# Optimization experiments

Measured on AMD Instinct MI355X. Metric: run time of the kernel, lower is better.

The kernel has to match this reference:

```python
import jax, jax.numpy as jnp
import numpy as np

# init kwargs baked in as constants
VTH_M = 0.5
VTH_S = 0.1
DECAY_M = 2.0
DECAY_S = 0.1
ALPHA = 4.0

B, T, C, H, W = 16, 32, 64, 32, 32


def spike_fn(x):
    # Heaviside spike; forward only (surrogate gradient used in bwd module)
    return jnp.where(x > 0, 1.0, 0.0).astype(x.dtype)


def setup_inputs() -> dict:
    key = jax.random.key(0)
    k1, k2, k3 = jax.random.split(key, 3)
    x = jax.random.normal(k1, (B, T, C, H, W), dtype=jnp.float32)
    vth_raw = jax.random.normal(k2, (C, H, W), dtype=jnp.float32)
    decay_raw = jax.random.normal(k3, (C, H, W), dtype=jnp.float32)
    return {"x": x, "vth_raw": vth_raw, "decay_raw": decay_raw}


def reference(x, vth_raw, decay_raw):
    # learned per-neuron threshold and decay
    vth = jax.nn.softplus(vth_raw * VTH_S + VTH_M) + 0.01          # (C,H,W)
    decay = jnp.clip(jax.nn.sigmoid(decay_raw * DECAY_S + DECAY_M), 0.0, 0.99)

    x_seq = jnp.moveaxis(x, 1, 0)  # (T, B, C, H, W)

    def scan_fn(v, x_t):
        v = v * decay + x_t                      # leaky integrate
        s = spike_fn(v - vth)                    # fire
        v = v - jax.lax.stop_gradient(s) * vth   # soft reset
        return v, s

    _, spikes = jax.lax.scan(scan_fn, jnp.zeros_like(x_seq[0]), x_seq)
    return jnp.moveaxis(spikes, 0, 1)  # (B, T, C, H, W)
```

## Files before the change

### kernel.cpp

```cpp
#include <hip/hip_runtime.h>
#include <math.h>


#define LIF_B    16
#define LIF_T    32
#define LIF_CHW  65536
#define LIF_CHW2 32768

typedef float vf2 __attribute__((ext_vector_type(2)));

__global__ __launch_bounds__(256) void HR_HLIFLayer2D_kernel(
    const float* __restrict__ x,
    const float* __restrict__ vth_raw,
    const float* __restrict__ decay_raw,
    float* __restrict__ out)
{
    const int g = blockIdx.x * 256 + threadIdx.x;
    const int b = g >> 15;
    const int j = g & (LIF_CHW2 - 1);

    const vf2 vr2 = reinterpret_cast<const vf2*>(vth_raw)[j];
    const vf2 dr2 = reinterpret_cast<const vf2*>(decay_raw)[j];
    const float vrr[2] = {vr2.x, vr2.y};
    const float drr[2] = {dr2.x, dr2.y};

    float vth[2], dec[2];
#pragma unroll
    for (int i = 0; i < 2; ++i) {
        float a  = __fmul_rn(vrr[i], 0.1f);
        float bb = __fadd_rn(a, 0.5f);
        double sp = log1p(exp((double)bb));
        vth[i] = __fadd_rn((float)sp, 0.01f);

        float z = __fmul_rn(drr[i], 0.1f);
        float w = __fadd_rn(z, 2.0f);
        double sg = 1.0 / (1.0 + exp(-(double)w));
        float sgf = (float)sg;
        sgf = fminf(fmaxf(sgf, 0.0f), 0.99f);
        dec[i] = sgf;
    }

    float v[2] = {0.f, 0.f};
    const size_t base2 = (size_t)b * (LIF_T * LIF_CHW2) + (size_t)j;
    const vf2* __restrict__ x2 = reinterpret_cast<const vf2*>(x);
    vf2* __restrict__ o2 = reinterpret_cast<vf2*>(out);

    vf2 xt = x2[base2];
#pragma unroll
    for (int t = 0; t < LIF_T; ++t) {
        const size_t idx = base2 + (size_t)t * LIF_CHW2;
        vf2 xn;
        if (t + 1 < LIF_T) xn = x2[idx + LIF_CHW2];

        const float xi[2] = {xt.x, xt.y};
        vf2 s;
        float so[2];
#pragma unroll
        for (int i = 0; i < 2; ++i) {
            float vv = __fadd_rn(__fmul_rn(v[i], dec[i]), xi[i]);
            float d = __fsub_rn(vv, vth[i]);
            bool fire = (d > 0.0f);
            so[i] = fire ? 1.0f : 0.0f;
            v[i] = fire ? d : vv;
        }
        s.x = so[0]; s.y = so[1];
        __builtin_nontemporal_store(s, &o2[idx]);
        xt = xn;
    }
}

extern "C" void kernel_launch(void* const* d_in, const int* in_sizes, int n_in,
                              void* d_out, int out_size, void* d_ws, size_t ws_size,
                              hipStream_t stream) {
    const float* x         = (const float*)d_in[0];
    const float* vth_raw   = (const float*)d_in[1];
    const float* decay_raw = (const float*)d_in[2];
    float* out             = (float*)d_out;

    const int total_threads = LIF_B * LIF_CHW2;
    const int block = 256;
    const int grid = total_threads / block;
    HR_HLIFLayer2D_kernel<<<grid, block, 0, stream>>>(x, vth_raw, decay_raw, out);
}
```

Measured before the change: 234.3 us.

## Precompute LIF params in a prepass kernel and widen to float4 nontemporal loads

A small prepass kernel computes the per-neuron threshold and decay (double-precision softplus/sigmoid) once into workspace, instead of having every batch thread recompute them. The main kernel then reads the precomputed values, switches from float2 to float4 vector accesses, and uses nontemporal loads for x. The trade-offs are an extra kernel launch, half as many threads (so less parallelism and more registers per thread), and a fallback path that still does the in-kernel computation when the workspace is too small.

```diff
diff --git a/kernel.cpp b/kernel.cpp
--- a/kernel.cpp
+++ b/kernel.cpp
@@ -5,66 +5,85 @@
 #define LIF_B    16
 #define LIF_T    32
 #define LIF_CHW  65536
-#define LIF_CHW2 32768
+#define LIF_CHW4 16384
 
-typedef float vf2 __attribute__((ext_vector_type(2)));
+typedef float vf4 __attribute__((ext_vector_type(4)));
 
+__device__ __forceinline__ float lif_vth_f(float raw) {
+    float a  = __fmul_rn(raw, 0.1f);
+    float bb = __fadd_rn(a, 0.5f);
+    double sp = log1p(exp((double)bb));
+    return __fadd_rn((float)sp, 0.01f);
+}
+
+__device__ __forceinline__ float lif_dec_f(float raw) {
+    float z = __fmul_rn(raw, 0.1f);
+    float w = __fadd_rn(z, 2.0f);
+    double sg = 1.0 / (1.0 + exp(-(double)w));
+    float sgf = (float)sg;
+    return fminf(fmaxf(sgf, 0.0f), 0.99f);
+}
+
+__global__ __launch_bounds__(256) void lif_params_kernel(
+    const float* __restrict__ vth_raw,
+    const float* __restrict__ decay_raw,
+    float* __restrict__ wp)
+{
+    const int i = blockIdx.x * 256 + threadIdx.x;
+    wp[i]           = lif_vth_f(vth_raw[i]);
+    wp[i + LIF_CHW] = lif_dec_f(decay_raw[i]);
+}
+
+template<bool PRE>
 __global__ __launch_bounds__(256) void HR_HLIFLayer2D_kernel(
     const float* __restrict__ x,
-    const float* __restrict__ vth_raw,
-    const float* __restrict__ decay_raw,
+    const float* __restrict__ p_vth,
+    const float* __restrict__ p_dec,
     float* __restrict__ out)
 {
     const int g = blockIdx.x * 256 + threadIdx.x;
-    const int b = g >> 15;
-    const int j = g & (LIF_CHW2 - 1);
+    const int b = g >> 14;
+    const int j = g & (LIF_CHW4 - 1);
 
-    const vf2 vr2 = reinterpret_cast<const vf2*>(vth_raw)[j];
-    const vf2 dr2 = reinterpret_cast<const vf2*>(decay_raw)[j];
-    const float vrr[2] = {vr2.x, vr2.y};
-    const float drr[2] = {dr2.x, dr2.y};
+    const vf4 rv = reinterpret_cast<const vf4*>(p_vth)[j];
+    const vf4 rd = reinterpret_cast<const vf4*>(p_dec)[j];
 
-    float vth[2], dec[2];
+    float vth[4], dec[4];
+    {
+        const float rva[4] = {rv.x, rv.y, rv.z, rv.w};
+        const float rda[4] = {rd.x, rd.y, rd.z, rd.w};
 #pragma unroll
-    for (int i = 0; i < 2; ++i) {
-        float a  = __fmul_rn(vrr[i], 0.1f);
-        float bb = __fadd_rn(a, 0.5f);
-        double sp = log1p(exp((double)bb));
-        vth[i] = __fadd_rn((float)sp, 0.01f);
-
-        float z = __fmul_rn(drr[i], 0.1f);
-        float w = __fadd_rn(z, 2.0f);
-        double sg = 1.0 / (1.0 + exp(-(double)w));
-        float sgf = (float)sg;
-        sgf = fminf(fmaxf(sgf, 0.0f), 0.99f);
-        dec[i] = sgf;
+        for (int i = 0; i < 4; ++i) {
+            vth[i] = PRE ? rva[i] : lif_vth_f(rva[i]);
+            dec[i] = PRE ? rda[i] : lif_dec_f(rda[i]);
+        }
     }
 
-    float v[2] = {0.f, 0.f};
-    const size_t base2 = (size_t)b * (LIF_T * LIF_CHW2) + (size_t)j;
-    const vf2* __restrict__ x2 = reinterpret_cast<const vf2*>(x);
-    vf2* __restrict__ o2 = reinterpret_cast<vf2*>(out);
+    float v[4] = {0.f, 0.f, 0.f, 0.f};
+    const size_t base4 = (size_t)b * (LIF_T * LIF_CHW4) + (size_t)j;
+    const vf4* __restrict__ x4 = reinterpret_cast<const vf4*>(x);
+    vf4* __restrict__ o4 = reinterpret_cast<vf4*>(out);
 
-    vf2 xt = x2[base2];
+    vf4 xt = __builtin_nontemporal_load(&x4[base4]);
 #pragma unroll
     for (int t = 0; t < LIF_T; ++t) {
-        const size_t idx = base2 + (size_t)t * LIF_CHW2;
-        vf2 xn;
-        if (t + 1 < LIF_T) xn = x2[idx + LIF_CHW2];
+        const size_t idx = base4 + (size_t)t * LIF_CHW4;
+        vf4 xn;
+        if (t + 1 < LIF_T)
+            xn = __builtin_nontemporal_load(&x4[idx + LIF_CHW4]);
 
-        const float xi[2] = {xt.x, xt.y};
-        vf2 s;
-        float so[2];
+        const float xi[4] = {xt.x, xt.y, xt.z, xt.w};
+        float so[4];
 #pragma unroll
-        for (int i = 0; i < 2; ++i) {
+        for (int i = 0; i < 4; ++i) {
             float vv = __fadd_rn(__fmul_rn(v[i], dec[i]), xi[i]);
             float d = __fsub_rn(vv, vth[i]);
-            bool fire = (d > 0.0f);
+            const bool fire = (d > 0.0f);
             so[i] = fire ? 1.0f : 0.0f;
             v[i] = fire ? d : vv;
         }
-        s.x = so[0]; s.y = so[1];
-        __builtin_nontemporal_store(s, &o2[idx]);
+        vf4 s; s.x = so[0]; s.y = so[1]; s.z = so[2]; s.w = so[3];
+        __builtin_nontemporal_store(s, &o4[idx]);
         xt = xn;
     }
 }
@@ -77,8 +96,13 @@
     const float* decay_raw = (const float*)d_in[2];
     float* out             = (float*)d_out;
 
-    const int total_threads = LIF_B * LIF_CHW2;
-    const int block = 256;
-    const int grid = total_threads / block;
-    HR_HLIFLayer2D_kernel<<<grid, block, 0, stream>>>(x, vth_raw, decay_raw, out);
+    const int grid = (LIF_B * LIF_CHW4) / 256;
+
+    if (ws_size >= (size_t)(2 * LIF_CHW * sizeof(float))) {
+        float* wp = (float*)d_ws;
+        lif_params_kernel<<<LIF_CHW / 256, 256, 0, stream>>>(vth_raw, decay_raw, wp);
+        HR_HLIFLayer2D_kernel<true><<<grid, 256, 0, stream>>>(x, wp, wp + LIF_CHW, out);
+    } else {
+        HR_HLIFLayer2D_kernel<false><<<grid, 256, 0, stream>>>(x, vth_raw, decay_raw, out);
+    }
 }
```

After: 231.8 us. About the same (-1.1%).
